# Kernel optimization log

Hardware: AMD Instinct MI355X
Metric: run time of the kernel (lower is better)

The kernel has to match this reference:

```python
import jax, jax.numpy as jnp
import numpy as np

EMBED_DIM = 512
NUM_HEADS = 8
HEAD_DIM = EMBED_DIM // NUM_HEADS
FFN_DIM = 4 * EMBED_DIM
B, S = 4, 2048
LN_EPS = 1e-5


def _linear_params(key, fan_in, fan_out):
    kw, kb = jax.random.split(key)
    bound = 1.0 / np.sqrt(fan_in)
    W = jax.random.uniform(kw, (fan_in, fan_out), jnp.float32, -bound, bound)
    b = jax.random.uniform(kb, (fan_out,), jnp.float32, -bound, bound)
    return W, b


def setup_inputs() -> dict:
    key = jax.random.key(0)
    ks = jax.random.split(key, 10)
    query = jax.random.normal(ks[0], (B, S, EMBED_DIM), jnp.float32)
    key_t = jax.random.normal(ks[1], (B, S, EMBED_DIM), jnp.float32)
    value = jax.random.normal(ks[2], (B, S, EMBED_DIM), jnp.float32)
    Wq, bq = _linear_params(ks[3], EMBED_DIM, EMBED_DIM)
    Wk, bk = _linear_params(ks[4], EMBED_DIM, EMBED_DIM)
    Wv, bv = _linear_params(ks[5], EMBED_DIM, EMBED_DIM)
    Wo, bo = _linear_params(ks[6], EMBED_DIM, EMBED_DIM)
    W1, b1 = _linear_params(ks[7], EMBED_DIM, FFN_DIM)
    W2, b2 = _linear_params(ks[8], FFN_DIM, EMBED_DIM)
    g1 = jnp.ones((EMBED_DIM,), jnp.float32); be1 = jnp.zeros((EMBED_DIM,), jnp.float32)
    g2 = jnp.ones((EMBED_DIM,), jnp.float32); be2 = jnp.zeros((EMBED_DIM,), jnp.float32)
    return dict(query=query, key=key_t, value=value,
                Wq=Wq, bq=bq, Wk=Wk, bk=bk, Wv=Wv, bv=bv, Wo=Wo, bo=bo,
                g1=g1, be1=be1, g2=g2, be2=be2,
                W1=W1, b1=b1, W2=W2, b2=b2)


def _layernorm(x, g, b):
    mu = jnp.mean(x, axis=-1, keepdims=True)
    var = jnp.mean(jnp.square(x - mu), axis=-1, keepdims=True)
    return (x - mu) * jax.lax.rsqrt(var + LN_EPS) * g + b


def reference(query, key, value, Wq, bq, Wk, bk, Wv, bv, Wo, bo,
              g1, be1, g2, be2, W1, b1, W2, b2):
    b_, s_ = query.shape[:2]
    # projections -> [B, H, S, Dh]
    Q = (query @ Wq + bq).reshape(b_, -1, NUM_HEADS, HEAD_DIM).transpose(0, 2, 1, 3)
    K = (key @ Wk + bk).reshape(b_, -1, NUM_HEADS, HEAD_DIM).transpose(0, 2, 1, 3)
    V = (value @ Wv + bv).reshape(b_, -1, NUM_HEADS, HEAD_DIM).transpose(0, 2, 1, 3)
    scores = jnp.einsum('bhqd,bhkd->bhqk', Q, K) / jnp.sqrt(jnp.float32(HEAD_DIM))
    attn = jax.nn.softmax(scores, axis=-1)  # dropout is eval-mode identity
    ctx = jnp.einsum('bhqk,bhkd->bhqd', attn, V)
    ctx = ctx.transpose(0, 2, 1, 3).reshape(b_, -1, EMBED_DIM)
    out = ctx @ Wo + bo
    out = _layernorm(query + out, g1, be1)
    ffn = jax.nn.gelu(out @ W1 + b1, approximate=False) @ W2 + b2
    return _layernorm(out + ffn, g2, be2)
```

## Files before the change

kernel.cpp:

```cpp
#include <hip/hip_runtime.h>
#include <hip/hip_bf16.h>
#include <math.h>

#define EMBED 512
#define NHEAD 8
#define HDIM 64
#define FFN 2048
#define BB 4
#define SS 2048
#define MROWS (BB*SS)
#define NB ((size_t)MROWS * EMBED)
#define LN_EPS 1e-5f
#define QSCALE 0.180336880111f

typedef __attribute__((ext_vector_type(8))) short short8;
typedef __attribute__((ext_vector_type(4))) float floatx4;

__device__ inline float bf2f(__hip_bfloat16 x) { return __bfloat162float(x); }
__device__ inline __hip_bfloat16 f2bf(float x) { return __float2bfloat16(x); }

__device__ inline float gelu_f(float x) {
    return 0.5f * x * (1.0f + erff(x * 0.70710678118654752f));
}

__device__ inline void async_copy16(const void* g, void* l) {
    __builtin_amdgcn_global_load_lds(
        (const __attribute__((address_space(1))) void*)g,
        (__attribute__((address_space(3))) void*)l, 16, 0, 0);
}

__device__ inline int sane_f(float v) {
    return (v == v) && (fabsf(v) > 0x1p-40f) && (fabsf(v) < 0x1p40f);
}

__global__ void detect_kernel(const void* __restrict__ q, int* __restrict__ flag) {
    const float* qf = (const float*)q;
    int lane = threadIdx.x;
    float v = qf[lane * 1024 + 7];
    bool ok = sane_f(v);
    unsigned long long m = __ballot(ok);
    if (lane == 0) *flag = (__popcll(m) >= 32) ? 1 : 0;
}

__global__ __launch_bounds__(256) void prep_kernel(
    const void* __restrict__ query, const void* __restrict__ keyi, const void* __restrict__ vali,
    const void* __restrict__ Wq, const void* __restrict__ Wk, const void* __restrict__ Wv,
    const void* __restrict__ Wo, const void* __restrict__ W1, const void* __restrict__ W2,
    const void* __restrict__ bq, const void* __restrict__ bk, const void* __restrict__ bv,
    const void* __restrict__ bo, const void* __restrict__ b1, const void* __restrict__ b2,
    const void* __restrict__ g1, const void* __restrict__ be1,
    const void* __restrict__ g2, const void* __restrict__ be2,
    __hip_bfloat16* __restrict__ qkvbf,
    __hip_bfloat16* __restrict__ Wcat,
    __hip_bfloat16* __restrict__ biasb)
{
    __shared__ __hip_bfloat16 L[64][65];
    const int f32 = sane_f(((const float*)query)[7]) + sane_f(((const float*)query)[1031]) +
                    sane_f(((const float*)query)[200003]) + sane_f(((const float*)query)[1000003]) >= 3;
    const int t = threadIdx.x;
    const int blk = blockIdx.x;

    if (blk < 6144) {
        size_t pos = ((size_t)blk * 256 + t) * 8;
        int sel = (int)(pos >> 22);
        size_t off = pos & (NB - 1);
        const void* src = sel == 0 ? query : sel == 1 ? keyi : vali;
        if (f32) {
            const float* s = (const float*)src + off;
            float4 f0 = *reinterpret_cast<const float4*>(s);
            float4 f1 = *reinterpret_cast<const float4*>(s + 4);
            alignas(16) __hip_bfloat16 h[8] = {
                f2bf(f0.x), f2bf(f0.y), f2bf(f0.z), f2bf(f0.w),
                f2bf(f1.x), f2bf(f1.y), f2bf(f1.z), f2bf(f1.w)};
            *reinterpret_cast<uint4*>(qkvbf + pos) = *reinterpret_cast<const uint4*>(h);
        } else {
            *reinterpret_cast<uint4*>(qkvbf + pos) =
                *reinterpret_cast<const uint4*>((const __hip_bfloat16*)src + off);
        }
        return;
    }

    const void* src; __hip_bfloat16* dst; int R, C, r0, c0;
    if (blk < 6400) {
        int b2i = blk - 6144; src = W1; dst = Wcat + 4 * 512 * 512;
        R = 512; C = 2048; r0 = (b2i >> 5) * 64; c0 = (b2i & 31) * 64;
    } else if (blk < 6656) {
        int b3 = blk - 6400; src = W2; dst = Wcat + 4 * 512 * 512 + 512 * 2048;
        R = 2048; C = 512; r0 = (b3 >> 3) * 64; c0 = (b3 & 7) * 64;
    } else if (blk < 6912) {
        int b4 = blk - 6656; int which = b4 >> 6; int tile = b4 & 63;
        src = which == 0 ? Wq : which == 1 ? Wk : which == 2 ? Wv : Wo;
        dst = Wcat + (size_t)which * 512 * 512;
        R = 512; C = 512; r0 = (tile >> 3) * 64; c0 = (tile & 7) * 64;
    } else {
        const void* srcs[10] = {bq, bk, bv, bo, b1, b2, g1, be1, g2, be2};
        const int offs[10] = {0, 512, 1024, 1536, 2048, 4096, 4608, 5120, 5632, 6144};
        const int lens[10] = {512, 512, 512, 512, 2048, 512, 512, 512, 512, 512};
        for (int a = 0; a < 10; ++a)
            for (int i = t; i < lens[a]; i += 256)
                biasb[offs[a] + i] = f32 ? f2bf(((const float*)srcs[a])[i])
                                         : ((const __hip_bfloat16*)srcs[a])[i];
        return;
    }
    for (int c = t; c < 4096; c += 256) {
        int lr = c >> 6, lc = c & 63;
        L[lr][lc] = f32 ? f2bf(((const float*)src)[(size_t)(r0 + lr) * C + c0 + lc])
                        : ((const __hip_bfloat16*)src)[(size_t)(r0 + lr) * C + c0 + lc];
    }
    __syncthreads();
    for (int c = t; c < 4096; c += 256) {
        int lr = c >> 6, lc = c & 63;
        dst[(size_t)(c0 + lr) * R + r0 + lc] = L[lc][lr];
    }
}

template<int ACT, int BIAS>
__global__ __launch_bounds__(256) void gemm_bt_lds_kernel(
    const __hip_bfloat16* __restrict__ A,
    const __hip_bfloat16* __restrict__ Bt,
    const __hip_bfloat16* __restrict__ bias,
    __hip_bfloat16* __restrict__ C,
    int M, int N, int K, int ksplit)
{
    const int bm = blockIdx.x * 128;
    const int bn = blockIdx.y * 128;
    int kbeg = 0, kend = K;
    if (BIAS == 0) {
        kbeg = blockIdx.z * ksplit;
        kend = kbeg + ksplit;
        C += (size_t)blockIdx.z * NB;
    }
    const int t = threadIdx.x;
    const int wave = t >> 6, lane = t & 63;
    const int wm = (wave >> 1) * 64, wn = (wave & 1) * 64;
    const int quad = lane >> 4, r = lane & 15;

    __shared__ alignas(16) __hip_bfloat16 As[2][128 * 32];
    __shared__ alignas(16) __hip_bfloat16 Bs[2][128 * 32];

    floatx4 acc[4][4];
    #pragma unroll
    for (int i = 0; i < 4; ++i)
        #pragma unroll
        for (int j = 0; j < 4; ++j)
            acc[i][j] = (floatx4){0.f, 0.f, 0.f, 0.f};

    const int c0 = wave * 128;

    for (int kt = kbeg; kt < kend; kt += 64) {
        #pragma unroll
        for (int h = 0; h < 2; ++h) {
            #pragma unroll
            for (int it = 0; it < 2; ++it) {
                int c = c0 + it * 64 + lane;
                int row = c >> 2, col = (c & 3) * 8;
                async_copy16(A + (size_t)(bm + row) * K + kt + h * 32 + col,
                             As[h] + (size_t)(c0 + it * 64) * 8);
                async_copy16(Bt + (size_t)(bn + row) * K + kt + h * 32 + col,
                             Bs[h] + (size_t)(c0 + it * 64) * 8);
            }
        }
        __syncthreads();
        #pragma unroll
        for (int h = 0; h < 2; ++h) {
            short8 af[4], bfr[4];
            #pragma unroll
            for (int i = 0; i < 4; ++i)
                af[i] = *reinterpret_cast<const short8*>(&As[h][(wm + i * 16 + r) * 32 + quad * 8]);
            #pragma unroll
            for (int j = 0; j < 4; ++j)
                bfr[j] = *reinterpret_cast<const short8*>(&Bs[h][(wn + j * 16 + r) * 32 + quad * 8]);
            #pragma unroll
            for (int i = 0; i < 4; ++i)
                #pragma unroll
                for (int j = 0; j < 4; ++j)
                    acc[i][j] = __builtin_amdgcn_mfma_f32_16x16x32_bf16(af[i], bfr[j], acc[i][j], 0, 0, 0);
        }
        __syncthreads();
    }

    #pragma unroll
    for (int j = 0; j < 4; ++j) {
        const int n = bn + wn + j * 16 + r;
        float bvv = BIAS ? bf2f(bias[n]) : 0.f;
        #pragma unroll
        for (int i = 0; i < 4; ++i) {
            #pragma unroll
            for (int v = 0; v < 4; ++v) {
                int m = bm + wm + i * 16 + quad * 4 + v;
                float x = acc[i][j][v] + bvv;
                if (ACT == 1) x = gelu_f(x);
                C[(size_t)m * N + n] = f2bf(x);
            }
        }
    }
}

__global__ __launch_bounds__(256) void gemm_qkv_fused_kernel(
    const __hip_bfloat16* __restrict__ Acat,
    const __hip_bfloat16* __restrict__ Wcat,
    const __hip_bfloat16* __restrict__ biascat,
    __hip_bfloat16* __restrict__ Ocat)
{
    const int sel = blockIdx.x >> 6;
    const __hip_bfloat16* A = Acat + (size_t)sel * NB;
    const __hip_bfloat16* Bt = Wcat + (size_t)sel * 512 * 512;
    const __hip_bfloat16* bias = biascat + sel * 512;
    __hip_bfloat16* C = Ocat + (size_t)sel * NB;

    const int bm = (blockIdx.x & 63) * 128;
    const int bn = blockIdx.y * 128;
    const int t = threadIdx.x;
    const int wave = t >> 6, lane = t & 63;
    const int wm = (wave >> 1) * 64, wn = (wave & 1) * 64;
    const int quad = lane >> 4, r = lane & 15;
    const int K = EMBED, N = EMBED;

    __shared__ alignas(16) __hip_bfloat16 As[2][128 * 32];
    __shared__ alignas(16) __hip_bfloat16 Bs[2][128 * 32];

    floatx4 acc[4][4];
    #pragma unroll
    for (int i = 0; i < 4; ++i)
        #pragma unroll
        for (int j = 0; j < 4; ++j)
            acc[i][j] = (floatx4){0.f, 0.f, 0.f, 0.f};

    const int c0 = wave * 128;

    for (int kt = 0; kt < K; kt += 64) {
        #pragma unroll
        for (int h = 0; h < 2; ++h) {
            #pragma unroll
            for (int it = 0; it < 2; ++it) {
                int c = c0 + it * 64 + lane;
                int row = c >> 2, col = (c & 3) * 8;
                async_copy16(A + (size_t)(bm + row) * K + kt + h * 32 + col,
                             As[h] + (size_t)(c0 + it * 64) * 8);
                async_copy16(Bt + (size_t)(bn + row) * K + kt + h * 32 + col,
                             Bs[h] + (size_t)(c0 + it * 64) * 8);
            }
        }
        __syncthreads();
        #pragma unroll
        for (int h = 0; h < 2; ++h) {
            short8 af[4], bfr[4];
            #pragma unroll
            for (int i = 0; i < 4; ++i)
                af[i] = *reinterpret_cast<const short8*>(&As[h][(wm + i * 16 + r) * 32 + quad * 8]);
            #pragma unroll
            for (int j = 0; j < 4; ++j)
                bfr[j] = *reinterpret_cast<const short8*>(&Bs[h][(wn + j * 16 + r) * 32 + quad * 8]);
            #pragma unroll
            for (int i = 0; i < 4; ++i)
                #pragma unroll
                for (int j = 0; j < 4; ++j)
                    acc[i][j] = __builtin_amdgcn_mfma_f32_16x16x32_bf16(af[i], bfr[j], acc[i][j], 0, 0, 0);
        }
        __syncthreads();
    }

    #pragma unroll
    for (int j = 0; j < 4; ++j) {
        const int n = bn + wn + j * 16 + r;
        const float bvv = bf2f(bias[n]);
        #pragma unroll
        for (int i = 0; i < 4; ++i) {
            #pragma unroll
            for (int v = 0; v < 4; ++v) {
                int m = bm + wm + i * 16 + quad * 4 + v;
                C[(size_t)m * N + n] = f2bf(acc[i][j][v] + bvv);
            }
        }
    }
}

__global__ __launch_bounds__(256) void vtrans_kernel(
    const __hip_bfloat16* __restrict__ Vb, __hip_bfloat16* __restrict__ Vt)
{
    const int bh = blockIdx.y;
    const int b = bh >> 3, h = bh & 7;
    const int s0 = blockIdx.x * 64;
    __shared__ alignas(16) __hip_bfloat16 L[64][72];
    const int t = threadIdx.x;
    for (int c = t; c < 512; c += 256) {
        int row = c >> 3, g = c & 7;
        *reinterpret_cast<uint4*>(&L[row][g * 8]) =
            *reinterpret_cast<const uint4*>(Vb + (size_t)(b * SS + s0 + row) * EMBED + h * 64 + g * 8);
    }
    __syncthreads();
    for (int c = t; c < 512; c += 256) {
        int d = c >> 3, g = c & 7;
        alignas(16) __hip_bfloat16 tmp[8];
        #pragma unroll
        for (int j = 0; j < 8; ++j) tmp[j] = L[g * 8 + j][d];
        *reinterpret_cast<uint4*>(Vt + ((size_t)bh * 64 + d) * SS + s0 + g * 8) =
            *reinterpret_cast<const uint4*>(tmp);
    }
}

__global__ __launch_bounds__(256) void attn_mfma_kernel(
    const __hip_bfloat16* __restrict__ Qg,
    const __hip_bfloat16* __restrict__ Kg,
    const __hip_bfloat16* __restrict__ Vt,
    __hip_bfloat16* __restrict__ ctx)
{
    const int bh = blockIdx.y;
    const int b = bh >> 3, h = bh & 7;
    const int q0 = blockIdx.x * 128;
    const int t = threadIdx.x;
    const int w = t >> 6, lane = t & 63;
    const int quad = lane >> 4, r = lane & 15;

    __shared__ alignas(16) __hip_bfloat16 Ks[2][2][64 * 32];
    __shared__ alignas(16) __hip_bfloat16 Vs[2][2][64 * 32];
    __shared__ alignas(16) __hip_bfloat16 Ps[4][32][72];

    const size_t bbase = (size_t)b * SS * EMBED;
    const size_t hoff = (size_t)h * HDIM;
    const size_t vtbase = (size_t)bh * HDIM * SS;

    short8 aq[2][2];
    #pragma unroll
    for (int s = 0; s < 2; ++s) {
        const __hip_bfloat16* qrow = Qg + bbase + (size_t)(q0 + w * 32 + s * 16 + r) * EMBED + hoff;
        short8 t0 = *reinterpret_cast<const short8*>(qrow + quad * 8);
        short8 t1 = *reinterpret_cast<const short8*>(qrow + 32 + quad * 8);
        #pragma unroll
        for (int i = 0; i < 8; ++i) {
            ((__hip_bfloat16*)&aq[s][0])[i] = f2bf(bf2f(((const __hip_bfloat16*)&t0)[i]) * QSCALE);
            ((__hip_bfloat16*)&aq[s][1])[i] = f2bf(bf2f(((const __hip_bfloat16*)&t1)[i]) * QSCALE);
        }
    }

    const short one = 0x3F80;
    const short8 bones = {one, one, one, one, one, one, one, one};

    const int tensor = w >> 1, slab = w & 1;
    const int srow = lane >> 2;
    const int scol = (((lane & 3) ^ ((srow >> 1) & 3)) * 8);
    const int cs = ((r >> 1) & 3) * 8;

    floatx4 o0[4], o1[4], l0a, l1a;
    #pragma unroll
    for (int nt = 0; nt < 4; ++nt) {
        o0[nt] = (floatx4){0.f, 0.f, 0.f, 0.f};
        o1[nt] = (floatx4){0.f, 0.f, 0.f, 0.f};
    }
    l0a = (floatx4){0.f, 0.f, 0.f, 0.f};
    l1a = (floatx4){0.f, 0.f, 0.f, 0.f};

    const __hip_bfloat16* kp[4];
    const __hip_bfloat16* vp[4];
    #pragma unroll
    for (int g = 0; g < 4; ++g) {
        int row = g * 16 + srow;
        kp[g] = Kg + bbase + (size_t)row * EMBED + hoff + slab * 32 + scol;
        vp[g] = Vt + vtbase + (size_t)row * SS + slab * 32 + scol;
    }

    if (tensor == 0) {
        #pragma unroll
        for (int g = 0; g < 4; ++g) {
            async_copy16(kp[g], &Ks[0][slab][g * 512]);
            kp[g] += 64 * EMBED;
        }
    } else {
        #pragma unroll
        for (int g = 0; g < 4; ++g) {
            async_copy16(vp[g], &Vs[0][slab][g * 512]);
            vp[g] += 64;
        }
    }
    __syncthreads();

    int cur = 0;
    for (int kt = 0; kt < SS; kt += 64) {
        if (kt + 64 < SS) {
            if (tensor == 0) {
                #pragma unroll
                for (int g = 0; g < 4; ++g) {
                    async_copy16(kp[g], &Ks[cur ^ 1][slab][g * 512]);
                    kp[g] += 64 * EMBED;
                }
            } else {
                #pragma unroll
                for (int g = 0; g < 4; ++g) {
                    async_copy16(vp[g], &Vs[cur ^ 1][slab][g * 512]);
                    vp[g] += 64;
                }
            }
        }

        floatx4 s0[4], s1[4];
        #pragma unroll
        for (int nt = 0; nt < 4; ++nt) {
            s0[nt] = (floatx4){0.f, 0.f, 0.f, 0.f};
            s1[nt] = (floatx4){0.f, 0.f, 0.f, 0.f};
        }
        __builtin_amdgcn_s_setprio(1);
        #pragma unroll
        for (int nt = 0; nt < 4; ++nt) {
            short8 ak0 = *reinterpret_cast<const short8*>(&Ks[cur][0][(nt * 16 + r) * 32 + (quad * 8 ^ cs)]);
            short8 ak1 = *reinterpret_cast<const short8*>(&Ks[cur][1][(nt * 16 + r) * 32 + (quad * 8 ^ cs)]);
            s0[nt] = __builtin_amdgcn_mfma_f32_16x16x32_bf16(ak0, aq[0][0], s0[nt], 0, 0, 0);
            s0[nt] = __builtin_amdgcn_mfma_f32_16x16x32_bf16(ak1, aq[0][1], s0[nt], 0, 0, 0);
            s1[nt] = __builtin_amdgcn_mfma_f32_16x16x32_bf16(ak0, aq[1][0], s1[nt], 0, 0, 0);
            s1[nt] = __builtin_amdgcn_mfma_f32_16x16x32_bf16(ak1, aq[1][1], s1[nt], 0, 0, 0);
        }
        __builtin_amdgcn_s_setprio(0);

        #pragma unroll
        for (int s = 0; s < 2; ++s) {
            floatx4* sc = s == 0 ? s0 : s1;
            #pragma unroll
            for (int nt = 0; nt < 4; ++nt) {
                float p0 = exp2f(sc[nt][0]), p1 = exp2f(sc[nt][1]);
                float p2 = exp2f(sc[nt][2]), p3 = exp2f(sc[nt][3]);
                __hip_bfloat162 pa = __float22bfloat162_rn(make_float2(p0, p1));
                __hip_bfloat162 pb = __float22bfloat162_rn(make_float2(p2, p3));
                uint2 u;
                u.x = *reinterpret_cast<unsigned*>(&pa);
                u.y = *reinterpret_cast<unsigned*>(&pb);
                *reinterpret_cast<uint2*>(&Ps[w][s * 16 + r][nt * 16 + quad * 4]) = u;
            }
        }

        short8 ap00 = *reinterpret_cast<const short8*>(&Ps[w][r][quad * 8]);
        short8 ap01 = *reinterpret_cast<const short8*>(&Ps[w][r][32 + quad * 8]);
        short8 ap10 = *reinterpret_cast<const short8*>(&Ps[w][16 + r][quad * 8]);
        short8 ap11 = *reinterpret_cast<const short8*>(&Ps[w][16 + r][32 + quad * 8]);
        __builtin_amdgcn_s_setprio(1);
        #pragma unroll
        for (int nt = 0; nt < 4; ++nt) {
            short8 bv0 = *reinterpret_cast<const short8*>(&Vs[cur][0][(nt * 16 + r) * 32 + (quad * 8 ^ cs)]);
            short8 bv1 = *reinterpret_cast<const short8*>(&Vs[cur][1][(nt * 16 + r) * 32 + (quad * 8 ^ cs)]);
            o0[nt] = __builtin_amdgcn_mfma_f32_16x16x32_bf16(ap00, bv0, o0[nt], 0, 0, 0);
            o0[nt] = __builtin_amdgcn_mfma_f32_16x16x32_bf16(ap01, bv1, o0[nt], 0, 0, 0);
            o1[nt] = __builtin_amdgcn_mfma_f32_16x16x32_bf16(ap10, bv0, o1[nt], 0, 0, 0);
            o1[nt] = __builtin_amdgcn_mfma_f32_16x16x32_bf16(ap11, bv1, o1[nt], 0, 0, 0);
        }
        l0a = __builtin_amdgcn_mfma_f32_16x16x32_bf16(ap00, bones, l0a, 0, 0, 0);
        l0a = __builtin_amdgcn_mfma_f32_16x16x32_bf16(ap01, bones, l0a, 0, 0, 0);
        l1a = __builtin_amdgcn_mfma_f32_16x16x32_bf16(ap10, bones, l1a, 0, 0, 0);
        l1a = __builtin_amdgcn_mfma_f32_16x16x32_bf16(ap11, bones, l1a, 0, 0, 0);
        __builtin_amdgcn_s_setprio(0);

        __syncthreads();
        cur ^= 1;
    }

    #pragma unroll
    for (int s = 0; s < 2; ++s) {
        floatx4* oa = s == 0 ? o0 : o1;
        floatx4 la = s == 0 ? l0a : l1a;
        #pragma unroll
        for (int v = 0; v < 4; ++v) {
            int q = q0 + w * 32 + s * 16 + quad * 4 + v;
            float inv = 1.0f / la[v];
            __hip_bfloat16* orow = ctx + bbase + (size_t)q * EMBED + hoff;
            #pragma unroll
            for (int nt = 0; nt < 4; ++nt)
                orow[nt * 16 + r] = f2bf(oa[nt][v] * inv);
        }
    }
}

template<int OUT32>
__global__ __launch_bounds__(256) void add_ln_split_kernel(
    const __hip_bfloat16* __restrict__ X,
    const __hip_bfloat16* __restrict__ Y0,
    const __hip_bfloat16* __restrict__ Y1,
    const __hip_bfloat16* __restrict__ bias,
    const __hip_bfloat16* __restrict__ g,
    const __hip_bfloat16* __restrict__ bt,
    void* __restrict__ out,
    const int* __restrict__ dflag)
{
    const int w = threadIdx.x >> 6, lane = threadIdx.x & 63;
    const int row = blockIdx.x * 4 + w;
    const size_t base = (size_t)row * EMBED + lane * 8;
    const int co = lane * 8;

    short8 xv  = *reinterpret_cast<const short8*>(X + base);
    short8 y0v = *reinterpret_cast<const short8*>(Y0 + base);
    short8 y1v = *reinterpret_cast<const short8*>(Y1 + base);
    short8 bv  = *reinterpret_cast<const short8*>(bias + co);

    float x[8];
    float s = 0.f;
    #pragma unroll
    for (int j = 0; j < 8; ++j) {
        x[j] = bf2f(((const __hip_bfloat16*)&xv)[j]) + bf2f(((const __hip_bfloat16*)&y0v)[j])
             + bf2f(((const __hip_bfloat16*)&y1v)[j]) + bf2f(((const __hip_bfloat16*)&bv)[j]);
        s += x[j];
    }
    #pragma unroll
    for (int off = 32; off; off >>= 1) s += __shfl_xor(s, off, 64);
    const float mu = s * (1.0f / EMBED);
    float vs = 0.f;
    #pragma unroll
    for (int j = 0; j < 8; ++j) { x[j] -= mu; vs += x[j] * x[j]; }
    #pragma unroll
    for (int off = 32; off; off >>= 1) vs += __shfl_xor(vs, off, 64);
    const float rstd = rsqrtf(vs * (1.0f / EMBED) + LN_EPS);

    short8 gv  = *reinterpret_cast<const short8*>(g + co);
    short8 btv = *reinterpret_cast<const short8*>(bt + co);
    if (OUT32 && *dflag) {
        float4 o0, o1;
        float of[8];
        #pragma unroll
        for (int j = 0; j < 8; ++j)
            of[j] = x[j] * rstd * bf2f(((const __hip_bfloat16*)&gv)[j]) + bf2f(((const __hip_bfloat16*)&btv)[j]);
        o0 = make_float4(of[0], of[1], of[2], of[3]);
        o1 = make_float4(of[4], of[5], of[6], of[7]);
        *reinterpret_cast<float4*>((float*)out + base) = o0;
        *reinterpret_cast<float4*>((float*)out + base + 4) = o1;
    } else {
        alignas(16) __hip_bfloat16 o[8];
        #pragma unroll
        for (int j = 0; j < 8; ++j)
            o[j] = f2bf(x[j] * rstd * bf2f(((const __hip_bfloat16*)&gv)[j]) + bf2f(((const __hip_bfloat16*)&btv)[j]));
        *reinterpret_cast<uint4*>((__hip_bfloat16*)out + base) = *reinterpret_cast<const uint4*>(o);
    }
}

extern "C" void kernel_launch(void* const* d_in, const int* in_sizes, int n_in,
                              void* d_out, int out_size, void* d_ws, size_t ws_size,
                              hipStream_t stream)
{
    (void)in_sizes; (void)n_in; (void)out_size; (void)ws_size;

    const void* query = d_in[0];
    const void* keyi  = d_in[1];
    const void* vali  = d_in[2];
    const void* Wq = d_in[3];  const void* bq = d_in[4];
    const void* Wk = d_in[5];  const void* bk = d_in[6];
    const void* Wv = d_in[7];  const void* bv = d_in[8];
    const void* Wo = d_in[9];  const void* bo = d_in[10];
    const void* g1 = d_in[11]; const void* be1 = d_in[12];
    const void* g2 = d_in[13]; const void* be2 = d_in[14];
    const void* W1 = d_in[15]; const void* b1 = d_in[16];
    const void* W2 = d_in[17]; const void* b2 = d_in[18];

    int* dflag = (int*)d_ws;
    __hip_bfloat16* biasb = (__hip_bfloat16*)((char*)d_ws + 64);
    __hip_bfloat16* Wcat = biasb + 8192;
    __hip_bfloat16* buf = Wcat + 4 * 512 * 512 + 2 * 512 * 2048;
    __hip_bfloat16* bqkvb = biasb;
    __hip_bfloat16* bob  = biasb + 1536;
    __hip_bfloat16* b1b  = biasb + 2048;
    __hip_bfloat16* b2b  = biasb + 4096;
    __hip_bfloat16* g1b  = biasb + 4608;
    __hip_bfloat16* be1b = biasb + 5120;
    __hip_bfloat16* g2b  = biasb + 5632;
    __hip_bfloat16* be2b = biasb + 6144;
    __hip_bfloat16* qkvbf  = buf;
    __hip_bfloat16* QKVo   = buf + 3 * NB;
    __hip_bfloat16* Qb = QKVo;
    __hip_bfloat16* Kb = QKVo + NB;
    __hip_bfloat16* Vb = QKVo + 2 * NB;
    __hip_bfloat16* Vt     = buf + 1 * NB;
    __hip_bfloat16* ctx    = buf + 2 * NB;
    __hip_bfloat16* Yw     = buf + 4 * NB;
    __hip_bfloat16* x1     = buf + 3 * NB;
    __hip_bfloat16* hbf    = buf + 4 * NB;
    __hip_bfloat16* Yf     = buf + 1 * NB;

    detect_kernel<<<1, 64, 0, stream>>>(query, dflag);

    prep_kernel<<<6913, 256, 0, stream>>>(
        query, keyi, vali, Wq, Wk, Wv, Wo, W1, W2,
        bq, bk, bv, bo, b1, b2, g1, be1, g2, be2,
        qkvbf, Wcat, biasb);

    gemm_qkv_fused_kernel<<<dim3(192, 4), 256, 0, stream>>>(qkvbf, Wcat, bqkvb, QKVo);

    vtrans_kernel<<<dim3(SS / 64, BB * NHEAD), 256, 0, stream>>>(Vb, Vt);

    attn_mfma_kernel<<<dim3(SS / 128, BB * NHEAD), 256, 0, stream>>>(
        Qb, Kb, Vt, ctx);

    gemm_bt_lds_kernel<0, 0><<<dim3(MROWS / 128, EMBED / 128, 2), 256, 0, stream>>>(
        ctx, Wcat + 3 * 512 * 512, nullptr, Yw, MROWS, EMBED, EMBED, EMBED / 2);
    add_ln_split_kernel<0><<<MROWS / 4, 256, 0, stream>>>(
        qkvbf, Yw, Yw + NB, bob, g1b, be1b, x1, dflag);

    gemm_bt_lds_kernel<1, 1><<<dim3(MROWS / 128, FFN / 128), 256, 0, stream>>>(
        x1, Wcat + 4 * 512 * 512, b1b, hbf, MROWS, FFN, EMBED, 0);
    gemm_bt_lds_kernel<0, 0><<<dim3(MROWS / 128, EMBED / 128, 2), 256, 0, stream>>>(
        hbf, Wcat + 4 * 512 * 512 + 512 * 2048, nullptr, Yf, MROWS, EMBED, FFN, FFN / 2);
    add_ln_split_kernel<1><<<MROWS / 4, 256, 0, stream>>>(
        x1, Yf, Yf + NB, b2b, g2b, be2b, d_out, dflag);
}
```

Baseline: 323.3 us.

## Fuse V transpose into QKV GEMM epilogue and add 256x256 FFN1 GEMM

```diff
diff --git a/kernel.cpp b/kernel.cpp
--- a/kernel.cpp
+++ b/kernel.cpp
@@ -200,7 +200,8 @@
     const __hip_bfloat16* __restrict__ Acat,
     const __hip_bfloat16* __restrict__ Wcat,
     const __hip_bfloat16* __restrict__ biascat,
-    __hip_bfloat16* __restrict__ Ocat)
+    __hip_bfloat16* __restrict__ Ocat,
+    __hip_bfloat16* __restrict__ Vt)
 {
     const int sel = blockIdx.x >> 6;
     const __hip_bfloat16* A = Acat + (size_t)sel * NB;
@@ -260,42 +261,120 @@
         __syncthreads();
     }
 
+    if (sel < 2) {
+        #pragma unroll
+        for (int j = 0; j < 4; ++j) {
+            const int n = bn + wn + j * 16 + r;
+            const float bvv = bf2f(bias[n]);
+            #pragma unroll
+            for (int i = 0; i < 4; ++i) {
+                #pragma unroll
+                for (int v = 0; v < 4; ++v) {
+                    int m = bm + wm + i * 16 + quad * 4 + v;
+                    C[(size_t)m * N + n] = f2bf(acc[i][j][v] + bvv);
+                }
+            }
+        }
+    } else {
+        #pragma unroll
+        for (int j = 0; j < 4; ++j) {
+            const int n = bn + wn + j * 16 + r;
+            const float bvv = bf2f(bias[n]);
+            const int hh = n >> 6, d = n & 63;
+            #pragma unroll
+            for (int i = 0; i < 4; ++i) {
+                int m0 = bm + wm + i * 16 + quad * 4;
+                int b = m0 >> 11, s0 = m0 & 2047;
+                alignas(8) __hip_bfloat16 o[4];
+                #pragma unroll
+                for (int v = 0; v < 4; ++v)
+                    o[v] = f2bf(acc[i][j][v] + bvv);
+                *reinterpret_cast<uint2*>(Vt + ((size_t)(b * 8 + hh) * 64 + d) * SS + s0) =
+                    *reinterpret_cast<const uint2*>(o);
+            }
+        }
+    }
+}
+
+__global__ __launch_bounds__(512, 2) void gemm_ffn1_256_kernel(
+    const __hip_bfloat16* __restrict__ A,
+    const __hip_bfloat16* __restrict__ Bt,
+    const __hip_bfloat16* __restrict__ bias,
+    __hip_bfloat16* __restrict__ C)
+{
+    const int bm = blockIdx.x * 256;
+    const int bn = blockIdx.y * 256;
+    const int K = EMBED, N = FFN;
+    const int t = threadIdx.x;
+    const int wave = t >> 6, lane = t & 63;
+    const int wmi = wave >> 2, wni = wave & 3;
+    const int wm = wmi * 128, wn = wni * 64;
+    const int quad = lane >> 4, r = lane & 15;
+
+    __shared__ alignas(16) __hip_bfloat16 As[2][2][256 * 32];
+    __shared__ alignas(16) __hip_bfloat16 Bs[2][2][256 * 32];
+
+    floatx4 acc[8][4];
+    #pragma unroll
+    for (int i = 0; i < 8; ++i)
+        #pragma unroll
+        for (int j = 0; j < 4; ++j)
+            acc[i][j] = (floatx4){0.f, 0.f, 0.f, 0.f};
+
+    auto stage = [&](int d, int kt) {
+        #pragma unroll
+        for (int h = 0; h < 2; ++h) {
+            #pragma unroll
+            for (int it = 0; it < 2; ++it) {
+                int c = wave * 128 + it * 64 + lane;
+                int row = c >> 2, col = (c & 3) * 8;
+                async_copy16(A + (size_t)(bm + row) * K + kt + h * 32 + col,
+                             As[d][h] + (size_t)(wave * 128 + it * 64) * 8);
+                async_copy16(Bt + (size_t)(bn + row) * K + kt + h * 32 + col,
+                             Bs[d][h] + (size_t)(wave * 128 + it * 64) * 8);
+            }
+        }
+    };
+
+    stage(0, 0);
+    __syncthreads();
+
+    int cur = 0;
+    for (int kt = 0; kt < K; kt += 64) {
+        if (kt + 64 < K) stage(cur ^ 1, kt + 64);
+        #pragma unroll
+        for (int h = 0; h < 2; ++h) {
+            short8 af[8], bfr[4];
+            #pragma unroll
+            for (int i = 0; i < 8; ++i)
+                af[i] = *reinterpret_cast<const short8*>(&As[cur][h][(wm + i * 16 + r) * 32 + quad * 8]);
+            #pragma unroll
+            for (int j = 0; j < 4; ++j)
+                bfr[j] = *reinterpret_cast<const short8*>(&Bs[cur][h][(wn + j * 16 + r) * 32 + quad * 8]);
+            __builtin_amdgcn_s_setprio(1);
+            #pragma unroll
+            for (int i = 0; i < 8; ++i)
+                #pragma unroll
+                for (int j = 0; j < 4; ++j)
+                    acc[i][j] = __builtin_amdgcn_mfma_f32_16x16x32_bf16(af[i], bfr[j], acc[i][j], 0, 0, 0);
+            __builtin_amdgcn_s_setprio(0);
+        }
+        __syncthreads();
+        cur ^= 1;
+    }
+
     #pragma unroll
     for (int j = 0; j < 4; ++j) {
         const int n = bn + wn + j * 16 + r;
         const float bvv = bf2f(bias[n]);
         #pragma unroll
-        for (int i = 0; i < 4; ++i) {
+        for (int i = 0; i < 8; ++i) {
             #pragma unroll
             for (int v = 0; v < 4; ++v) {
                 int m = bm + wm + i * 16 + quad * 4 + v;
-                C[(size_t)m * N + n] = f2bf(acc[i][j][v] + bvv);
-            }
-        }
-    }
-}
-
-__global__ __launch_bounds__(256) void vtrans_kernel(
-    const __hip_bfloat16* __restrict__ Vb, __hip_bfloat16* __restrict__ Vt)
-{
-    const int bh = blockIdx.y;
-    const int b = bh >> 3, h = bh & 7;
-    const int s0 = blockIdx.x * 64;
-    __shared__ alignas(16) __hip_bfloat16 L[64][72];
-    const int t = threadIdx.x;
-    for (int c = t; c < 512; c += 256) {
-        int row = c >> 3, g = c & 7;
-        *reinterpret_cast<uint4*>(&L[row][g * 8]) =
-            *reinterpret_cast<const uint4*>(Vb + (size_t)(b * SS + s0 + row) * EMBED + h * 64 + g * 8);
-    }
-    __syncthreads();
-    for (int c = t; c < 512; c += 256) {
-        int d = c >> 3, g = c & 7;
-        alignas(16) __hip_bfloat16 tmp[8];
-        #pragma unroll
-        for (int j = 0; j < 8; ++j) tmp[j] = L[g * 8 + j][d];
-        *reinterpret_cast<uint4*>(Vt + ((size_t)bh * 64 + d) * SS + s0 + g * 8) =
-            *reinterpret_cast<const uint4*>(tmp);
+                C[(size_t)m * N + n] = f2bf(gelu_f(acc[i][j][v] + bvv));
+            }
+        }
     }
 }
 
@@ -560,8 +639,7 @@
     __hip_bfloat16* QKVo   = buf + 3 * NB;
     __hip_bfloat16* Qb = QKVo;
     __hip_bfloat16* Kb = QKVo + NB;
-    __hip_bfloat16* Vb = QKVo + 2 * NB;
-    __hip_bfloat16* Vt     = buf + 1 * NB;
+    __hip_bfloat16* Vt     = buf + 6 * NB;
     __hip_bfloat16* ctx    = buf + 2 * NB;
     __hip_bfloat16* Yw     = buf + 4 * NB;
     __hip_bfloat16* x1     = buf + 3 * NB;
@@ -575,9 +653,7 @@
         bq, bk, bv, bo, b1, b2, g1, be1, g2, be2,
         qkvbf, Wcat, biasb);
 
-    gemm_qkv_fused_kernel<<<dim3(192, 4), 256, 0, stream>>>(qkvbf, Wcat, bqkvb, QKVo);
-
-    vtrans_kernel<<<dim3(SS / 64, BB * NHEAD), 256, 0, stream>>>(Vb, Vt);
+    gemm_qkv_fused_kernel<<<dim3(192, 4), 256, 0, stream>>>(qkvbf, Wcat, bqkvb, QKVo, Vt);
 
     attn_mfma_kernel<<<dim3(SS / 128, BB * NHEAD), 256, 0, stream>>>(
         Qb, Kb, Vt, ctx);
@@ -587,8 +663,8 @@
     add_ln_split_kernel<0><<<MROWS / 4, 256, 0, stream>>>(
         qkvbf, Yw, Yw + NB, bob, g1b, be1b, x1, dflag);
 
-    gemm_bt_lds_kernel<1, 1><<<dim3(MROWS / 128, FFN / 128), 256, 0, stream>>>(
-        x1, Wcat + 4 * 512 * 512, b1b, hbf, MROWS, FFN, EMBED, 0);
+    gemm_ffn1_256_kernel<<<dim3(MROWS / 256, FFN / 256), 512, 0, stream>>>(
+        x1, Wcat + 4 * 512 * 512, b1b, hbf);
     gemm_bt_lds_kernel<0, 0><<<dim3(MROWS / 128, EMBED / 128, 2), 256, 0, stream>>>(
         hbf, Wcat + 4 * 512 * 512 + 512 * 2048, nullptr, Yf, MROWS, EMBED, FFN, FFN / 2);
     add_ln_split_kernel<1><<<MROWS / 4, 256, 0, stream>>>(
```

New measurement: 335.0 us. 3.6% more time.

## Fuse V transpose into QKV GEMM epilogue and fold dtype detect into prep

Applied to the files above, without the earlier changes.

```diff
diff --git a/kernel.cpp b/kernel.cpp
--- a/kernel.cpp
+++ b/kernel.cpp
@@ -33,15 +33,6 @@
     return (v == v) && (fabsf(v) > 0x1p-40f) && (fabsf(v) < 0x1p40f);
 }
 
-__global__ void detect_kernel(const void* __restrict__ q, int* __restrict__ flag) {
-    const float* qf = (const float*)q;
-    int lane = threadIdx.x;
-    float v = qf[lane * 1024 + 7];
-    bool ok = sane_f(v);
-    unsigned long long m = __ballot(ok);
-    if (lane == 0) *flag = (__popcll(m) >= 32) ? 1 : 0;
-}
-
 __global__ __launch_bounds__(256) void prep_kernel(
     const void* __restrict__ query, const void* __restrict__ keyi, const void* __restrict__ vali,
     const void* __restrict__ Wq, const void* __restrict__ Wk, const void* __restrict__ Wv,
@@ -52,7 +43,8 @@
     const void* __restrict__ g2, const void* __restrict__ be2,
     __hip_bfloat16* __restrict__ qkvbf,
     __hip_bfloat16* __restrict__ Wcat,
-    __hip_bfloat16* __restrict__ biasb)
+    __hip_bfloat16* __restrict__ biasb,
+    int* __restrict__ dflag)
 {
     __shared__ __hip_bfloat16 L[64][65];
     const int f32 = sane_f(((const float*)query)[7]) + sane_f(((const float*)query)[1031]) +
@@ -93,6 +85,7 @@
         dst = Wcat + (size_t)which * 512 * 512;
         R = 512; C = 512; r0 = (tile >> 3) * 64; c0 = (tile & 7) * 64;
     } else {
+        if (t == 0) *dflag = f32 ? 1 : 0;
         const void* srcs[10] = {bq, bk, bv, bo, b1, b2, g1, be1, g2, be2};
         const int offs[10] = {0, 512, 1024, 1536, 2048, 4096, 4608, 5120, 5632, 6144};
         const int lens[10] = {512, 512, 512, 512, 2048, 512, 512, 512, 512, 512};
@@ -200,7 +193,8 @@
     const __hip_bfloat16* __restrict__ Acat,
     const __hip_bfloat16* __restrict__ Wcat,
     const __hip_bfloat16* __restrict__ biascat,
-    __hip_bfloat16* __restrict__ Ocat)
+    __hip_bfloat16* __restrict__ Ocat,
+    __hip_bfloat16* __restrict__ Vt)
 {
     const int sel = blockIdx.x >> 6;
     const __hip_bfloat16* A = Acat + (size_t)sel * NB;
@@ -260,42 +254,38 @@
         __syncthreads();
     }
 
-    #pragma unroll
-    for (int j = 0; j < 4; ++j) {
-        const int n = bn + wn + j * 16 + r;
-        const float bvv = bf2f(bias[n]);
-        #pragma unroll
-        for (int i = 0; i < 4; ++i) {
-            #pragma unroll
-            for (int v = 0; v < 4; ++v) {
-                int m = bm + wm + i * 16 + quad * 4 + v;
-                C[(size_t)m * N + n] = f2bf(acc[i][j][v] + bvv);
-            }
-        }
-    }
-}
-
-__global__ __launch_bounds__(256) void vtrans_kernel(
-    const __hip_bfloat16* __restrict__ Vb, __hip_bfloat16* __restrict__ Vt)
-{
-    const int bh = blockIdx.y;
-    const int b = bh >> 3, h = bh & 7;
-    const int s0 = blockIdx.x * 64;
-    __shared__ alignas(16) __hip_bfloat16 L[64][72];
-    const int t = threadIdx.x;
-    for (int c = t; c < 512; c += 256) {
-        int row = c >> 3, g = c & 7;
-        *reinterpret_cast<uint4*>(&L[row][g * 8]) =
-            *reinterpret_cast<const uint4*>(Vb + (size_t)(b * SS + s0 + row) * EMBED + h * 64 + g * 8);
-    }
-    __syncthreads();
-    for (int c = t; c < 512; c += 256) {
-        int d = c >> 3, g = c & 7;
-        alignas(16) __hip_bfloat16 tmp[8];
-        #pragma unroll
-        for (int j = 0; j < 8; ++j) tmp[j] = L[g * 8 + j][d];
-        *reinterpret_cast<uint4*>(Vt + ((size_t)bh * 64 + d) * SS + s0 + g * 8) =
-            *reinterpret_cast<const uint4*>(tmp);
+    if (sel < 2) {
+        #pragma unroll
+        for (int j = 0; j < 4; ++j) {
+            const int n = bn + wn + j * 16 + r;
+            const float bvv = bf2f(bias[n]);
+            #pragma unroll
+            for (int i = 0; i < 4; ++i) {
+                #pragma unroll
+                for (int v = 0; v < 4; ++v) {
+                    int m = bm + wm + i * 16 + quad * 4 + v;
+                    C[(size_t)m * N + n] = f2bf(acc[i][j][v] + bvv);
+                }
+            }
+        }
+    } else {
+        #pragma unroll
+        for (int j = 0; j < 4; ++j) {
+            const int n = bn + wn + j * 16 + r;
+            const float bvv = bf2f(bias[n]);
+            const int hh = n >> 6, d = n & 63;
+            #pragma unroll
+            for (int i = 0; i < 4; ++i) {
+                int m0 = bm + wm + i * 16 + quad * 4;
+                int b = m0 >> 11, s0 = m0 & 2047;
+                alignas(8) __hip_bfloat16 o[4];
+                #pragma unroll
+                for (int v = 0; v < 4; ++v)
+                    o[v] = f2bf(acc[i][j][v] + bvv);
+                *reinterpret_cast<uint2*>(Vt + ((size_t)(b * 8 + hh) * 64 + d) * SS + s0) =
+                    *reinterpret_cast<const uint2*>(o);
+            }
+        }
     }
 }
 
@@ -560,24 +550,19 @@
     __hip_bfloat16* QKVo   = buf + 3 * NB;
     __hip_bfloat16* Qb = QKVo;
     __hip_bfloat16* Kb = QKVo + NB;
-    __hip_bfloat16* Vb = QKVo + 2 * NB;
-    __hip_bfloat16* Vt     = buf + 1 * NB;
+    __hip_bfloat16* Vt     = buf + 6 * NB;
     __hip_bfloat16* ctx    = buf + 2 * NB;
     __hip_bfloat16* Yw     = buf + 4 * NB;
     __hip_bfloat16* x1     = buf + 3 * NB;
     __hip_bfloat16* hbf    = buf + 4 * NB;
     __hip_bfloat16* Yf     = buf + 1 * NB;
 
-    detect_kernel<<<1, 64, 0, stream>>>(query, dflag);
-
     prep_kernel<<<6913, 256, 0, stream>>>(
         query, keyi, vali, Wq, Wk, Wv, Wo, W1, W2,
         bq, bk, bv, bo, b1, b2, g1, be1, g2, be2,
-        qkvbf, Wcat, biasb);
-
-    gemm_qkv_fused_kernel<<<dim3(192, 4), 256, 0, stream>>>(qkvbf, Wcat, bqkvb, QKVo);
-
-    vtrans_kernel<<<dim3(SS / 64, BB * NHEAD), 256, 0, stream>>>(Vb, Vt);
+        qkvbf, Wcat, biasb, dflag);
+
+    gemm_qkv_fused_kernel<<<dim3(192, 4), 256, 0, stream>>>(qkvbf, Wcat, bqkvb, QKVo, Vt);
 
     attn_mfma_kernel<<<dim3(SS / 128, BB * NHEAD), 256, 0, stream>>>(
         Qb, Kb, Vt, ctx);
```

Result: no change. 319.5 us, median of 3 (-1.2%).
